# Optimization experiments

Hardware: AMD Instinct MI355X
Metric: run time of the kernel (lower is better)

## Reference

```python
import jax, jax.numpy as jnp
import numpy as np

# (left, right, top, bottom) zero-pad offsets for the 8 neighbors (matches nn.ZeroPad2d order in source)
PADS = [(0, 2, 0, 2), (1, 1, 0, 2), (2, 0, 0, 2), (0, 2, 1, 1),
        (2, 0, 1, 1), (0, 2, 2, 0), (1, 1, 2, 0), (2, 0, 2, 0)]
CROP_H = [96, 128, 160, 192]
CROP_W = [192, 256, 320, 384]
PROP_TIME = 3


def _shift_pad8(x):
    # x: [B,1,h,w] -> [B,8,h+2,w+2], each channel a differently shifted zero-padded copy
    xs = [jnp.pad(x[:, 0], ((0, 0), (t, b), (l, r))) for (l, r, t, b) in PADS]
    return jnp.stack(xs, axis=1)


def _cspn(guidance, blur_depth, sparse_depth):
    # guidance: [B,8,h,w]; blur_depth/sparse_depth: [B,1,h,w]. norm_type='8sum'.
    gates = [jnp.pad(guidance[:, k], ((0, 0), (t, b), (l, r)))
             for k, (l, r, t, b) in enumerate(PADS)]
    gate_wb = jnp.stack(gates, axis=1)                              # [B,8,h+2,w+2]
    abs_weight = jnp.sum(jnp.abs(gate_wb), axis=1, keepdims=True)   # [B,1,h+2,w+2]
    gate_wb = gate_wb / abs_weight
    gate_sum = jnp.sum(gate_wb, axis=1, keepdims=True)[:, :, 1:-1, 1:-1]  # [B,1,h,w]

    sparse_mask = jnp.sign(sparse_depth)
    raw = blur_depth
    result = blur_depth
    for i in range(PROP_TIME):
        if i == 0:
            result = (1.0 - sparse_mask) * result + sparse_mask * sparse_depth
        neigh = jnp.sum(gate_wb * _shift_pad8(result), axis=1, keepdims=True)
        result = (1.0 - gate_sum) * raw + neigh[:, :, 1:-1, 1:-1]
    return result


def _conv_block(x, w, b):
    # ConvBlock (monodepth2 style): reflection pad 1 + 3x3 conv + ELU
    xp = jnp.pad(x, ((0, 0), (0, 0), (1, 1), (1, 1)), mode='reflect')
    y = jax.lax.conv_general_dilated(xp, w, (1, 1), 'VALID',
                                     dimension_numbers=('NCHW', 'OIHW', 'NCHW'))
    return jax.nn.elu(y + b[None, :, None, None])


def _center_crop(x, h, w):
    oh, ow = x.shape[2], x.shape[3]
    hs = max(int(round((oh - h) / 2)), 0)
    ws = max(int(round((ow - w) / 2)), 0)
    return x[:, :, hs:min(hs + h, oh), ws:min(ws + w, ow)]


def _stage_pad(depth, h, w):
    hs, ws = depth.shape[2], depth.shape[3]
    ph, pw = (h - hs) // 2, (w - ws) // 2
    return jnp.pad(depth, ((0, 0), (0, 0), (ph, ph), (pw, pw)))


def _masked_median(x, mask):
    # torch.median semantics: lower median of the masked elements
    s = jnp.sort(jnp.where(mask, x, jnp.inf).ravel())
    n = jnp.sum(mask)
    return jnp.take(s, (n - 1) // 2)


def _stage_forward(features, rgbd, dep_last, w, b, h, wd):
    rgbd_c = _center_crop(rgbd, h, wd)
    feat_c = _center_crop(features, h, wd)
    dep = rgbd_c[:, 0:1]                       # channel 0, as in source
    mask = jnp.sign(dep_last)
    dep_fusion = dep_last * mask + dep * (1.0 - mask)
    guided_map = _conv_block(feat_c, w, b)     # [B,8,h,wd]
    x = _cspn(guided_map, dep_fusion, dep_last)
    return jnp.clip(x, 0.0, 1.0)


def setup_inputs() -> dict:
    key = jax.random.key(0)
    ks = jax.random.split(key, 12)
    B, H, W = 16, 256, 512
    inp = {
        'features': jax.random.normal(ks[0], (B, 16, H, W), jnp.float32),
        'blur_depth': jax.random.uniform(ks[1], (B, 1, H, W), jnp.float32),
        'gt': jax.random.uniform(ks[2], (B, 1, H, W), jnp.float32),
        'rgb': jax.random.uniform(ks[3], (B, 3, H, W), jnp.float32),
        'stage': jnp.arange(4, dtype=jnp.int64 if jax.config.jax_enable_x64 else jnp.int32),
    }
    scale = 1.0 / np.sqrt(16 * 9)
    for i in range(4):
        inp[f'w{i}'] = jax.random.normal(ks[4 + i], (8, 16, 3, 3), jnp.float32) * scale
        inp[f'b{i}'] = jax.random.normal(ks[8 + i], (8,), jnp.float32) * 0.01
    return inp


def reference(features, blur_depth, gt, rgb, w0, b0, w1, b1, w2, b2, w3, b3, stage):
    stage_list = [int(s) for s in np.asarray(stage)]
    gt_pos = gt > 0
    scale = _masked_median(gt, gt_pos) / _masked_median(blur_depth, gt_pos)
    all_scale = gt / blur_depth
    blur_depth_o = blur_depth * scale
    gt = jnp.where((all_scale > 1.2) | (all_scale < 0.8), 0.0, gt)
    rgbd = jnp.concatenate([rgb, blur_depth_o], axis=1)
    dep_last = _center_crop(gt, 96, 192)

    params = [(w0, b0), (w1, b1), (w2, b2), (w3, b3)]
    out = None
    for index, i in enumerate(stage_list):
        w, b = params[i]
        if index == len(stage_list) - 1:
            out = _stage_forward(features, rgbd, dep_last, w, b, CROP_H[i], CROP_W[i])
        else:
            ref_last = jax.lax.stop_gradient(
                _stage_forward(features, rgbd, dep_last, w, b, CROP_H[i], CROP_W[i]))
            dep_last = _stage_pad(ref_last, CROP_H[i + 1], CROP_W[i + 1])
    return out
```

## Files before the change

kernel.cpp:

```cpp
#include <hip/hip_runtime.h>
#include <math.h>


#define B 16
#define FH 256
#define FW 512
#define TH 32
#define TW 32
#define HALO 3
#define LD 38
#define GD 36
#define MAXC 6

typedef __attribute__((ext_vector_type(8))) short short8;
typedef __attribute__((ext_vector_type(4))) float f32x4;

__device__ __forceinline__ int swzslot(int cc, int h) {
  return (((cc << 1) | h) ^ (cc & 1) ^ ((cc >> 1) & 2));
}

__global__ __launch_bounds__(256) void prep_all_kernel(
    const float* __restrict__ gt, const float* __restrict__ blur,
    const float* __restrict__ rgb, const float* __restrict__ w0c,
    const float* __restrict__ w1c, const float* __restrict__ w2c,
    const float* __restrict__ w3c, short8* __restrict__ wf,
    float* __restrict__ r0, float* __restrict__ r1, float* __restrict__ r2,
    float* __restrict__ r3) {
  if (blockIdx.x == 0 && threadIdx.x < 64) {
    int lane = threadIdx.x;
    int px = lane & 15, g = lane >> 4;
    const float* Ws[4] = {w0c, w1c, w2c, w3c};
    for (int st = 0; st < 4; ++st) {
      const float* wgt = Ws[st];
      for (int t = 0; t < 5; ++t) {
        short8 wh, wl;
        for (int j = 0; j < 8; ++j) {
          int k = 32 * t + 8 * g + j;
          int s = k >> 4, ci = k & 15;
          float wv = 0.0f;
          if (px < 8 && s < 9) wv = wgt[(px * 16 + ci) * 9 + s];
          uint uw = __float_as_uint(wv);
          uint hw_ = (uw + 0x8000u) & 0xFFFF0000u;
          float wlo = wv - __uint_as_float(hw_);
          wh[j] = (short)(hw_ >> 16);
          wl[j] = (short)((__float_as_uint(wlo) + 0x8000u) >> 16);
        }
        wf[((st * 5 + t) * 2 + 0) * 64 + lane] = wh;
        wf[((st * 5 + t) * 2 + 1) * 64 + lane] = wl;
      }
    }
  }

  int idx = blockIdx.x * blockDim.x + threadIdx.x;
  const int n0 = B * 96 * 192, n1 = B * 128 * 256, n2 = B * 160 * 320,
            n3 = B * 192 * 384;
  float* dst;
  int h, w, hs, ws;
  if (idx < n0) {
    dst = r0; h = 96; w = 192; hs = 80; ws = 160;
  } else if (idx < n0 + n1) {
    idx -= n0; dst = r1; h = 128; w = 256; hs = 64; ws = 128;
  } else if (idx < n0 + n1 + n2) {
    idx -= n0 + n1; dst = r2; h = 160; w = 320; hs = 48; ws = 96;
  } else if (idx < n0 + n1 + n2 + n3) {
    idx -= n0 + n1 + n2; dst = r3; h = 192; w = 384; hs = 32; ws = 64;
  } else {
    return;
  }
  int x = idx % w;
  int t = idx / w;
  int y = t % h;
  int b = t / h;
  size_t g = (size_t)b * FH * FW + (size_t)(hs + y) * FW + (ws + x);
  float dep = rgb[((size_t)b * 3) * FH * FW + (size_t)(hs + y) * FW + (ws + x)];
  if (dst == r0) {
    float gv = gt[g];
    float s = gv / blur[g];
    float dl = (s > 1.2f || s < 0.8f) ? 0.0f : gv;
    dst[idx] = (dl > 0.0f) ? dl : dep;
  } else {
    dst[idx] = dep;
  }
}

__global__ __launch_bounds__(256) void conv_mfma_kernel(
    const float* __restrict__ feat, const short8* __restrict__ wf,
    const float* __restrict__ b0c, float* __restrict__ g0,
    const float* __restrict__ b1c, float* __restrict__ g1,
    const float* __restrict__ b2c, float* __restrict__ g2,
    const float* __restrict__ b3c, float* __restrict__ g3) {
  __shared__ uint4 sH[18 * 72];
  __shared__ uint4 sL[18 * 72];

  int bid = blockIdx.x;
  int bx = bid % 12;
  int t0 = bid / 12;
  int by = t0 % 12;
  int b = t0 / 12;
  int ty0 = by << 4, tx0 = bx << 5;

  int tid = threadIdx.x;
  int lane = tid & 63, wv = tid >> 6;
  int px = lane & 15, g = lane >> 4;
  int h_ = g & 1, gb = g >> 1;

  const size_t FHW = (size_t)FH * FW;
  const float* fb = feat + (size_t)b * 16 * FHW;
  for (int u = tid; u < 612; u += 256) {
    int rr = u / 34, cc = u % 34;
    int yy = ty0 + rr - 1;
    yy = (yy < 0) ? 0 : ((yy > 191) ? 191 : yy);
    int xx = tx0 + cc - 1;
    xx = (xx < 0) ? 0 : ((xx > 383) ? 383 : xx);
    const float* fp = fb + (size_t)(32 + yy) * FW + (64 + xx);
    uint hiD[8], loD[8];
#pragma unroll
    for (int i = 0; i < 8; ++i) {
      float a0 = fp[(size_t)(2 * i) * FHW];
      float a1 = fp[(size_t)(2 * i + 1) * FHW];
      uint u0 = __float_as_uint(a0), u1 = __float_as_uint(a1);
      uint h0 = (u0 + 0x8000u) & 0xFFFF0000u;
      uint h1 = (u1 + 0x8000u) & 0xFFFF0000u;
      float l0 = a0 - __uint_as_float(h0);
      float l1 = a1 - __uint_as_float(h1);
      hiD[i] = (h0 >> 16) | h1;
      loD[i] = ((__float_as_uint(l0) + 0x8000u) >> 16) |
               (((__float_as_uint(l1) + 0x8000u) >> 16) << 16);
    }
    int r72 = rr * 72;
    sH[r72 + swzslot(cc, 0)] = make_uint4(hiD[0], hiD[1], hiD[2], hiD[3]);
    sH[r72 + swzslot(cc, 1)] = make_uint4(hiD[4], hiD[5], hiD[6], hiD[7]);
    sL[r72 + swzslot(cc, 0)] = make_uint4(loD[0], loD[1], loD[2], loD[3]);
    sL[r72 + swzslot(cc, 1)] = make_uint4(loD[4], loD[5], loD[6], loD[7]);
  }
  __syncthreads();

  const short8* pH = (const short8*)sH;
  const short8* pL = (const short8*)sL;
  const int dyE_[5] = {-1, -1, 0, 1, 1};
  const int dxE_[5] = {-1, 1, 0, -1, 1};
  const int dyO_[5] = {-1, 0, 0, 1, 0};
  const int dxO_[5] = {0, -1, 1, 0, 0};

  const int SH[4] = {96, 128, 160, 192};
  const int SW[4] = {192, 256, 320, 384};
  const int OY[4] = {48, 32, 16, 0};
  const int OX[4] = {96, 64, 32, 0};
  const float* BIAS[4] = {b0c, b1c, b2c, b3c};
  float* GD_[4] = {g0, g1, g2, g3};

#pragma unroll
  for (int st = 0; st < 4; ++st) {
    int sh = SH[st], sw = SW[st], oy = OY[st], ox = OX[st];
    bool inR = (ty0 >= oy) && (ty0 + 16 <= oy + sh) && (tx0 >= ox) &&
               (tx0 + 32 <= ox + sw);
    if (!inR) continue;
    bool topE = (ty0 == oy), botE = (ty0 + 16 == oy + sh);
    bool leftE = (tx0 == ox), rightE = (tx0 + 32 == ox + sw);

    const short8* wfs = wf + st * 640;
    short8 WH[5], WL[5];
#pragma unroll
    for (int t = 0; t < 5; ++t) {
      WH[t] = wfs[(t * 2 + 0) * 64 + lane];
      WL[t] = wfs[(t * 2 + 1) * 64 + lane];
    }
    float bias4[4];
    {
      const float* bp = BIAS[st] + ((g & 1) << 2);
#pragma unroll
      for (int r = 0; r < 4; ++r) bias4[r] = bp[r];
    }
    size_t hw = (size_t)sh * sw;
    float* guid = GD_[st];

    for (int i = 0; i < 8; ++i) {
      int tau = wv * 8 + i;
      int row = tau >> 1, xt = tau & 1;
      int rr0 = row + 1;
      int cc0 = (xt << 4) + px + 1;
      f32x4 acc = {bias4[0], bias4[1], bias4[2], bias4[3]};
#pragma unroll
      for (int t = 0; t < 5; ++t) {
        int dy = gb ? dyO_[t] : dyE_[t];
        int dx = gb ? dxO_[t] : dxE_[t];
        int rr = rr0 + dy;
        if (dy < 0 && topE && row == 0) rr = rr0 + 1;
        if (dy > 0 && botE && row == 15) rr = rr0 - 1;
        int cc = cc0 + dx;
        if (dx < 0 && leftE && cc0 == 1) cc = cc0 + 1;
        if (dx > 0 && rightE && cc0 == 32) cc = cc0 - 1;
        int idx = rr * 72 + swzslot(cc, h_);
        short8 fh = pH[idx];
        short8 fl = pL[idx];
        acc = __builtin_amdgcn_mfma_f32_16x16x32_bf16(WH[t], fh, acc, 0, 0, 0);
        acc = __builtin_amdgcn_mfma_f32_16x16x32_bf16(WH[t], fl, acc, 0, 0, 0);
        acc = __builtin_amdgcn_mfma_f32_16x16x32_bf16(WL[t], fh, acc, 0, 0, 0);
      }
      if (g < 2) {
        int ly = ty0 + row - oy, lx = tx0 + (xt << 4) + px - ox;
        float* gp = guid + (size_t)b * 8 * hw + (size_t)ly * sw + lx;
#pragma unroll
        for (int r = 0; r < 4; ++r) {
          int oo = g * 4 + r;
          float v = acc[r];
          v = (v > 0.0f) ? v : (__expf(v) - 1.0f);
          gp[(size_t)oo * hw] = v;
        }
      }
    }
  }
}

__global__ __launch_bounds__(256) void cspn3_kernel(
    const float* __restrict__ guid, const float* __restrict__ raw,
    const float* __restrict__ rgb, float* __restrict__ dst, int h, int w,
    int hs, int wss, int h2, int w2, int ph, int pw, int last) {
  __shared__ float sraw[LD * LD];
  __shared__ float s0[LD * LD];
  __shared__ float s1[LD * LD];

  int tpw = w / TW, tph = h / TH;
  int tile = blockIdx.x;
  int tx = tile % tpw;
  int t2 = tile / tpw;
  int ty = t2 % tph;
  int b = t2 / tph;
  int oy = ty * TH - HALO, ox = tx * TW - HALO;
  int tid = threadIdx.x;

  const float* rb = raw + (size_t)b * h * w;

  for (int e = tid; e < LD * LD; e += 256) {
    int r = e / LD, c = e % LD;
    int gy = oy + r, gx = ox + c;
    bool in = (gy >= 0 && gy < h && gx >= 0 && gx < w);
    sraw[e] = in ? rb[(size_t)gy * w + gx] : 0.0f;
  }
  __syncthreads();

  const int dy8[8] = {1, 1, 1, 0, 0, -1, -1, -1};
  const int dx8[8] = {1, 0, -1, 1, -1, 1, 0, -1};
  const int off8[8] = {LD + 1, LD, LD - 1, 1, -1, -LD + 1, -LD, -LD - 1};

  const float* gb = guid + (size_t)b * 8 * h * w;
  float cg[MAXC][8];
  float r0[MAXC];
  int adr[MAXC];
#pragma unroll
  for (int ch = 0; ch < MAXC; ++ch) {
    int p = tid + ch * 256;
    bool ok = p < GD * GD;
    int pp = ok ? p : 0;
    int py = pp / GD + 1, px = pp % GD + 1;
    adr[ch] = py * LD + px;
    int gy = oy + py, gx = ox + px;
    bool in = ok && gy >= 0 && gy < h && gx >= 0 && gx < w;
    float wsum = 0.0f, asum = 0.0f;
    float g[8];
#pragma unroll
    for (int k = 0; k < 8; ++k) {
      int ny = gy + dy8[k], nx = gx + dx8[k];
      bool nin = ok && ny >= 0 && ny < h && nx >= 0 && nx < w;
      float gk = nin ? gb[(size_t)k * h * w + (size_t)ny * w + nx] : 0.0f;
      g[k] = gk;
      wsum += gk;
      asum += fabsf(gk);
    }
    float inv = in ? (1.0f / asum) : 0.0f;
#pragma unroll
    for (int k = 0; k < 8; ++k) cg[ch][k] = g[k] * inv;
    r0[ch] = in ? (1.0f - wsum * inv) * sraw[adr[ch]] : 0.0f;
  }

#pragma unroll
  for (int ch = 0; ch < MAXC; ++ch) {
    int p = tid + ch * 256;
    if (p < GD * GD) {
      float v = r0[ch];
#pragma unroll
      for (int k = 0; k < 8; ++k) v += cg[ch][k] * sraw[adr[ch] + off8[k]];
      s0[adr[ch]] = v;
    }
  }
  __syncthreads();

#pragma unroll
  for (int ch = 0; ch < MAXC; ++ch) {
    int p = tid + ch * 256;
    if (p < GD * GD) {
      int py = p / GD + 1, px = p % GD + 1;
      if (py >= 2 && py <= 35 && px >= 2 && px <= 35) {
        float v = r0[ch];
#pragma unroll
        for (int k = 0; k < 8; ++k) v += cg[ch][k] * s0[adr[ch] + off8[k]];
        s1[adr[ch]] = v;
      }
    }
  }
  __syncthreads();

#pragma unroll
  for (int ch = 0; ch < MAXC; ++ch) {
    int p = tid + ch * 256;
    if (p < GD * GD) {
      int py = p / GD + 1, px = p % GD + 1;
      if (py >= 3 && py <= 34 && px >= 3 && px <= 34) {
        float v = r0[ch];
#pragma unroll
        for (int k = 0; k < 8; ++k) v += cg[ch][k] * s1[adr[ch] + off8[k]];
        float dl = fminf(fmaxf(v, 0.0f), 1.0f);
        int gy = oy + py, gx = ox + px;
        if (last) {
          dst[((size_t)b * h + gy) * w + gx] = dl;
        } else {
          float dep = rgb[((size_t)b * 3) * FH * FW + (size_t)(hs + gy) * FW +
                          (wss + gx)];
          dst[((size_t)b * h2 + (gy + ph)) * w2 + (gx + pw)] =
              (dl > 0.0f) ? dl : dep;
        }
      }
    }
  }
}

extern "C" void kernel_launch(void* const* d_in, const int* in_sizes, int n_in,
                              void* d_out, int out_size, void* d_ws,
                              size_t ws_size, hipStream_t stream) {
  (void)in_sizes; (void)n_in; (void)out_size; (void)ws_size;
  const float* feat = (const float*)d_in[0];
  const float* blur = (const float*)d_in[1];
  const float* gt = (const float*)d_in[2];
  const float* rgb = (const float*)d_in[3];
  const float* W[4] = {(const float*)d_in[5], (const float*)d_in[7],
                       (const float*)d_in[9], (const float*)d_in[11]};
  const float* Bs[4] = {(const float*)d_in[6], (const float*)d_in[8],
                        (const float*)d_in[10], (const float*)d_in[12]};
  float* out = (float*)d_out;

  float* G0 = (float*)d_ws;
  float* G1 = G0 + (size_t)B * 8 * 96 * 192;
  float* G2 = G1 + (size_t)B * 8 * 128 * 256;
  float* G3 = G2 + (size_t)B * 8 * 160 * 320;
  float* RAW[4];
  RAW[0] = G3 + (size_t)B * 8 * 192 * 384;
  RAW[1] = RAW[0] + (size_t)B * 96 * 192;
  RAW[2] = RAW[1] + (size_t)B * 128 * 256;
  RAW[3] = RAW[2] + (size_t)B * 160 * 320;
  short8* WF = (short8*)(RAW[3] + (size_t)B * 192 * 384);
  float* G[4] = {G0, G1, G2, G3};

  const int CH[4] = {96, 128, 160, 192};
  const int CW[4] = {192, 256, 320, 384};

  {
    int n = B * (96 * 192 + 128 * 256 + 160 * 320 + 192 * 384);
    prep_all_kernel<<<(n + 255) / 256, 256, 0, stream>>>(
        gt, blur, rgb, W[0], W[1], W[2], W[3], WF, RAW[0], RAW[1], RAW[2],
        RAW[3]);
  }

  conv_mfma_kernel<<<2304, 256, 0, stream>>>(feat, WF, Bs[0], G0, Bs[1], G1,
                                             Bs[2], G2, Bs[3], G3);

  for (int i = 0; i < 4; ++i) {
    int h = CH[i], w = CW[i];
    int hs = (FH - h) / 2, wss = (FW - w) / 2;
    int ntiles = B * (h / TH) * (w / TW);
    if (i < 3) {
      int h2 = CH[i + 1], w2 = CW[i + 1];
      int ph = (h2 - h) / 2, pw = (w2 - w) / 2;
      cspn3_kernel<<<ntiles, 256, 0, stream>>>(G[i], RAW[i], rgb, RAW[i + 1],
                                               h, w, hs, wss, h2, w2, ph, pw,
                                               0);
    } else {
      cspn3_kernel<<<ntiles, 256, 0, stream>>>(G[i], RAW[i], rgb, out, h, w,
                                               hs, wss, h, w, 0, 0, 1);
    }
  }
}
```

Before: 173.2 us.

## Drop full RAW prefill, read rgb border directly in CSPN; precompute conv offsets

The prep kernel no longer fills the stage 1-3 raw buffers with rgb depth. It only computes stage 0. Each CSPN kernel now reads the border ring (outside the previous stage's written region) straight from rgb, which avoids a large write and reread of those buffers. The conv kernel also switches the bf16 hi/lo split from rounding to truncation and precomputes the neighbour shared-memory indices per row and column. Truncation changes the split error slightly, but the hi+lo sum stays close, so this should not change results meaningfully.

```diff
diff --git a/kernel.cpp b/kernel.cpp
--- a/kernel.cpp
+++ b/kernel.cpp
@@ -24,8 +24,7 @@
     const float* __restrict__ rgb, const float* __restrict__ w0c,
     const float* __restrict__ w1c, const float* __restrict__ w2c,
     const float* __restrict__ w3c, short8* __restrict__ wf,
-    float* __restrict__ r0, float* __restrict__ r1, float* __restrict__ r2,
-    float* __restrict__ r3) {
+    float* __restrict__ r0) {
   if (blockIdx.x == 0 && threadIdx.x < 64) {
     int lane = threadIdx.x;
     int px = lane & 15, g = lane >> 4;
@@ -52,35 +51,19 @@
   }
 
   int idx = blockIdx.x * blockDim.x + threadIdx.x;
-  const int n0 = B * 96 * 192, n1 = B * 128 * 256, n2 = B * 160 * 320,
-            n3 = B * 192 * 384;
-  float* dst;
-  int h, w, hs, ws;
-  if (idx < n0) {
-    dst = r0; h = 96; w = 192; hs = 80; ws = 160;
-  } else if (idx < n0 + n1) {
-    idx -= n0; dst = r1; h = 128; w = 256; hs = 64; ws = 128;
-  } else if (idx < n0 + n1 + n2) {
-    idx -= n0 + n1; dst = r2; h = 160; w = 320; hs = 48; ws = 96;
-  } else if (idx < n0 + n1 + n2 + n3) {
-    idx -= n0 + n1 + n2; dst = r3; h = 192; w = 384; hs = 32; ws = 64;
-  } else {
-    return;
-  }
+  const int n0 = B * 96 * 192;
+  if (idx >= n0) return;
+  const int h = 96, w = 192, hs = 80, ws = 160;
   int x = idx % w;
   int t = idx / w;
   int y = t % h;
   int b = t / h;
   size_t g = (size_t)b * FH * FW + (size_t)(hs + y) * FW + (ws + x);
   float dep = rgb[((size_t)b * 3) * FH * FW + (size_t)(hs + y) * FW + (ws + x)];
-  if (dst == r0) {
-    float gv = gt[g];
-    float s = gv / blur[g];
-    float dl = (s > 1.2f || s < 0.8f) ? 0.0f : gv;
-    dst[idx] = (dl > 0.0f) ? dl : dep;
-  } else {
-    dst[idx] = dep;
-  }
+  float gv = gt[g];
+  float s = gv / blur[g];
+  float dl = (s > 1.2f || s < 0.8f) ? 0.0f : gv;
+  r0[idx] = (dl > 0.0f) ? dl : dep;
 }
 
 __global__ __launch_bounds__(256) void conv_mfma_kernel(
@@ -119,13 +102,13 @@
       float a0 = fp[(size_t)(2 * i) * FHW];
       float a1 = fp[(size_t)(2 * i + 1) * FHW];
       uint u0 = __float_as_uint(a0), u1 = __float_as_uint(a1);
-      uint h0 = (u0 + 0x8000u) & 0xFFFF0000u;
-      uint h1 = (u1 + 0x8000u) & 0xFFFF0000u;
+      uint h0 = u0 & 0xFFFF0000u;
+      uint h1 = u1 & 0xFFFF0000u;
       float l0 = a0 - __uint_as_float(h0);
       float l1 = a1 - __uint_as_float(h1);
       hiD[i] = (h0 >> 16) | h1;
-      loD[i] = ((__float_as_uint(l0) + 0x8000u) >> 16) |
-               (((__float_as_uint(l1) + 0x8000u) >> 16) << 16);
+      loD[i] = (__float_as_uint(l0) >> 16) |
+               (__float_as_uint(l1) & 0xFFFF0000u);
     }
     int r72 = rr * 72;
     sH[r72 + swzslot(cc, 0)] = make_uint4(hiD[0], hiD[1], hiD[2], hiD[3]);
@@ -137,10 +120,6 @@
 
   const short8* pH = (const short8*)sH;
   const short8* pL = (const short8*)sL;
-  const int dyE_[5] = {-1, -1, 0, 1, 1};
-  const int dxE_[5] = {-1, 1, 0, -1, 1};
-  const int dyO_[5] = {-1, 0, 0, 1, 0};
-  const int dxO_[5] = {0, -1, 1, 0, 0};
 
   const int SH[4] = {96, 128, 160, 192};
   const int SW[4] = {192, 256, 320, 384};
@@ -174,23 +153,34 @@
     size_t hw = (size_t)sh * sw;
     float* guid = GD_[st];
 
+    int csl[2][3];
+#pragma unroll
+    for (int xt = 0; xt < 2; ++xt) {
+      int cc0 = (xt << 4) + px + 1;
+      int ccm = (leftE && cc0 == 1) ? cc0 + 1 : cc0 - 1;
+      int ccp = (rightE && cc0 == 32) ? cc0 - 1 : cc0 + 1;
+      csl[xt][0] = swzslot(ccm, h_);
+      csl[xt][1] = swzslot(cc0, h_);
+      csl[xt][2] = swzslot(ccp, h_);
+    }
+
+#pragma unroll
     for (int i = 0; i < 8; ++i) {
       int tau = wv * 8 + i;
-      int row = tau >> 1, xt = tau & 1;
+      int row = tau >> 1;
+      const int xt = i & 1;
       int rr0 = row + 1;
-      int cc0 = (xt << 4) + px + 1;
+      int rm = (topE && row == 0) ? rr0 + 1 : rr0 - 1;
+      int rp = (botE && row == 15) ? rr0 - 1 : rr0 + 1;
+      int rbm = rm * 72, rb_ = rr0 * 72, rbp = rp * 72;
+      const int c0 = csl[xt][0], c1 = csl[xt][1], c2 = csl[xt][2];
+      int iE[5] = {rbm + c0, rbm + c2, rb_ + c1, rbp + c0, rbp + c2};
+      int iO[5] = {rbm + c1, rb_ + c0, rb_ + c2, rbp + c1, rb_ + c1};
+
       f32x4 acc = {bias4[0], bias4[1], bias4[2], bias4[3]};
 #pragma unroll
       for (int t = 0; t < 5; ++t) {
-        int dy = gb ? dyO_[t] : dyE_[t];
-        int dx = gb ? dxO_[t] : dxE_[t];
-        int rr = rr0 + dy;
-        if (dy < 0 && topE && row == 0) rr = rr0 + 1;
-        if (dy > 0 && botE && row == 15) rr = rr0 - 1;
-        int cc = cc0 + dx;
-        if (dx < 0 && leftE && cc0 == 1) cc = cc0 + 1;
-        if (dx > 0 && rightE && cc0 == 32) cc = cc0 - 1;
-        int idx = rr * 72 + swzslot(cc, h_);
+        int idx = gb ? iO[t] : iE[t];
         short8 fh = pH[idx];
         short8 fl = pL[idx];
         acc = __builtin_amdgcn_mfma_f32_16x16x32_bf16(WH[t], fh, acc, 0, 0, 0);
@@ -215,7 +205,8 @@
 __global__ __launch_bounds__(256) void cspn3_kernel(
     const float* __restrict__ guid, const float* __restrict__ raw,
     const float* __restrict__ rgb, float* __restrict__ dst, int h, int w,
-    int hs, int wss, int h2, int w2, int ph, int pw, int last) {
+    int hs, int wss, int h2, int w2, int ph, int pw, int last, int py0,
+    int py1, int px0, int px1) {
   __shared__ float sraw[LD * LD];
   __shared__ float s0[LD * LD];
   __shared__ float s1[LD * LD];
@@ -230,12 +221,19 @@
   int tid = threadIdx.x;
 
   const float* rb = raw + (size_t)b * h * w;
+  const float* rgb0 = rgb + ((size_t)b * 3) * FH * FW;
 
   for (int e = tid; e < LD * LD; e += 256) {
     int r = e / LD, c = e % LD;
     int gy = oy + r, gx = ox + c;
     bool in = (gy >= 0 && gy < h && gx >= 0 && gx < w);
-    sraw[e] = in ? rb[(size_t)gy * w + gx] : 0.0f;
+    float v = 0.0f;
+    if (in) {
+      bool prev = (gy >= py0 && gy < py1 && gx >= px0 && gx < px1);
+      v = prev ? rb[(size_t)gy * w + gx]
+               : rgb0[(size_t)(hs + gy) * FW + (wss + gx)];
+    }
+    sraw[e] = v;
   }
   __syncthreads();
 
@@ -314,8 +312,7 @@
         if (last) {
           dst[((size_t)b * h + gy) * w + gx] = dl;
         } else {
-          float dep = rgb[((size_t)b * 3) * FH * FW + (size_t)(hs + gy) * FW +
-                          (wss + gx)];
+          float dep = rgb0[(size_t)(hs + gy) * FW + (wss + gx)];
           dst[((size_t)b * h2 + (gy + ph)) * w2 + (gx + pw)] =
               (dl > 0.0f) ? dl : dep;
         }
@@ -353,12 +350,8 @@
   const int CH[4] = {96, 128, 160, 192};
   const int CW[4] = {192, 256, 320, 384};
 
-  {
-    int n = B * (96 * 192 + 128 * 256 + 160 * 320 + 192 * 384);
-    prep_all_kernel<<<(n + 255) / 256, 256, 0, stream>>>(
-        gt, blur, rgb, W[0], W[1], W[2], W[3], WF, RAW[0], RAW[1], RAW[2],
-        RAW[3]);
-  }
+  prep_all_kernel<<<1152, 256, 0, stream>>>(gt, blur, rgb, W[0], W[1], W[2],
+                                            W[3], WF, RAW[0]);
 
   conv_mfma_kernel<<<2304, 256, 0, stream>>>(feat, WF, Bs[0], G0, Bs[1], G1,
                                              Bs[2], G2, Bs[3], G3);
@@ -367,15 +360,18 @@
     int h = CH[i], w = CW[i];
     int hs = (FH - h) / 2, wss = (FW - w) / 2;
     int ntiles = B * (h / TH) * (w / TW);
+    int py0 = 0, py1 = h, px0 = 0, px1 = w;
+    if (i > 0) { py0 = 16; py1 = h - 16; px0 = 32; px1 = w - 32; }
     if (i < 3) {
       int h2 = CH[i + 1], w2 = CW[i + 1];
       int ph = (h2 - h) / 2, pw = (w2 - w) / 2;
       cspn3_kernel<<<ntiles, 256, 0, stream>>>(G[i], RAW[i], rgb, RAW[i + 1],
                                                h, w, hs, wss, h2, w2, ph, pw,
-                                               0);
+                                               0, py0, py1, px0, px1);
     } else {
       cspn3_kernel<<<ntiles, 256, 0, stream>>>(G[i], RAW[i], rgb, out, h, w,
-                                               hs, wss, h, w, 0, 0, 1);
-    }
-  }
-}
+                                               hs, wss, h, w, 0, 0, 1, py0,
+                                               py1, px0, px1);
+    }
+  }
+}
```

Measured after the change: 163.2 us. 1.06x faster.
